# Kernel optimization log

Measured on AMD Instinct MI355X. Metric: run time of the kernel, lower is better.

Reference implementation:

```python
import jax, jax.numpy as jnp
import numpy as np

FEATS = 1024
HEAD = 16
MLP_HIDDEN = 4096
HEAD_DIM = FEATS // HEAD
SQRT_D = float(FEATS) ** 0.5  # module scales by sqrt(feats), not sqrt(head_dim)
LN_EPS = 1e-5


def layer_norm(x, g, b):
    mu = jnp.mean(x, axis=-1, keepdims=True)
    var = jnp.mean(jnp.square(x - mu), axis=-1, keepdims=True)
    return (x - mu) * jax.lax.rsqrt(var + LN_EPS) * g + b


def setup_inputs() -> dict:
    key = jax.random.key(0)
    ks = jax.random.split(key, 12)
    s = 1.0 / np.sqrt(FEATS)
    s2 = 1.0 / np.sqrt(MLP_HIDDEN)
    return {
        "x": jax.random.normal(ks[0], (2, 2048, FEATS), dtype=jnp.float32),
        "ln1_g": jnp.ones((FEATS,), jnp.float32),
        "ln1_b": jnp.zeros((FEATS,), jnp.float32),
        "wq": jax.random.normal(ks[1], (FEATS, FEATS), jnp.float32) * s,
        "bq": jnp.zeros((FEATS,), jnp.float32),
        "wk": jax.random.normal(ks[2], (FEATS, FEATS), jnp.float32) * s,
        "bk": jnp.zeros((FEATS,), jnp.float32),
        "wv": jax.random.normal(ks[3], (FEATS, FEATS), jnp.float32) * s,
        "bv": jnp.zeros((FEATS,), jnp.float32),
        "wo": jax.random.normal(ks[4], (FEATS, FEATS), jnp.float32) * s,
        "bo": jnp.zeros((FEATS,), jnp.float32),
        "ln2_g": jnp.ones((FEATS,), jnp.float32),
        "ln2_b": jnp.zeros((FEATS,), jnp.float32),
        "w1": jax.random.normal(ks[5], (MLP_HIDDEN, FEATS), jnp.float32) * s,
        "b1": jnp.zeros((MLP_HIDDEN,), jnp.float32),
        "w2": jax.random.normal(ks[6], (FEATS, MLP_HIDDEN), jnp.float32) * s2,
        "b2": jnp.zeros((FEATS,), jnp.float32),
    }


def reference(x, ln1_g, ln1_b, wq, bq, wk, bk, wv, bv, wo, bo,
              ln2_g, ln2_b, w1, b1, w2, b2):
    b, n, f = x.shape
    h = layer_norm(x, ln1_g, ln1_b)
    # qkv projections (torch Linear: y = x @ W.T + b)
    q = (h @ wq.T + bq).reshape(b, n, HEAD, HEAD_DIM).transpose(0, 2, 1, 3)
    k = (h @ wk.T + bk).reshape(b, n, HEAD, HEAD_DIM).transpose(0, 2, 1, 3)
    v = (h @ wv.T + bv).reshape(b, n, HEAD, HEAD_DIM).transpose(0, 2, 1, 3)
    score = jax.nn.softmax(jnp.einsum('bhif,bhjf->bhij', q, k) / SQRT_D, axis=-1)
    attn = jnp.einsum('bhij,bhjf->bihf', score, v).reshape(b, n, f)
    o = attn @ wo.T + bo
    out1 = o + x
    h2 = layer_norm(out1, ln2_g, ln2_b)
    mlp = jax.nn.relu(jax.nn.relu(h2 @ w1.T + b1) @ w2.T + b2)
    return mlp + out1
```

## Files before the change

kernel.cpp:

```cpp
#include <hip/hip_runtime.h>
#include <hip/hip_bf16.h>

#define FEATS 1024
#define NH 16
#define HD 64
#define SEQ 2048
#define BATCH 2
#define MTOT (BATCH*SEQ)
#define MLPH 4096

typedef __attribute__((ext_vector_type(8))) short bf16x8;
typedef __attribute__((ext_vector_type(4))) float f32x4;

static_assert(sizeof(bf16x8) == 16, "bf16x8 must be 16B");

__device__ __forceinline__ unsigned short f2bf(float f) {
    unsigned int u = __float_as_uint(f);
    unsigned int lsb = (u >> 16) & 1u;
    u += 0x7fffu + lsb;
    return (unsigned short)(u >> 16);
}

#define ASYNC16(GP, LP) __builtin_amdgcn_global_load_lds( \
    (const __attribute__((address_space(1))) void*)(GP),  \
    (__attribute__((address_space(3))) void*)(LP), 16, 0, 0)

__global__ __launch_bounds__(256) void cvt_kernel(const float* __restrict__ src,
                                                  unsigned short* __restrict__ dst, int n) {
    int i = (blockIdx.x * 256 + threadIdx.x) * 4;
    if (i + 3 < n) {
        float4 v = *(const float4*)(src + i);
        ushort4 o;
        o.x = f2bf(v.x); o.y = f2bf(v.y); o.z = f2bf(v.z); o.w = f2bf(v.w);
        *(ushort4*)(dst + i) = o;
    }
}

__global__ __launch_bounds__(256) void concat3_kernel(const float* __restrict__ a,
                                                      const float* __restrict__ b,
                                                      const float* __restrict__ c,
                                                      float* __restrict__ o) {
    int i = blockIdx.x * 256 + threadIdx.x;
    float v = (i < 1024) ? a[i] : ((i < 2048) ? b[i - 1024] : c[i - 2048]);
    o[i] = v;
}

__global__ __launch_bounds__(256) void ln_kernel(const float* __restrict__ x,
                                                 const float* __restrict__ g,
                                                 const float* __restrict__ bta,
                                                 unsigned short* __restrict__ h) {
    __shared__ float red[8];
    const int row = blockIdx.x;
    const int t = threadIdx.x;
    const float* xr = x + (size_t)row * FEATS;
    float4 v = ((const float4*)xr)[t];
    float s  = v.x + v.y + v.z + v.w;
    float ss = v.x * v.x + v.y * v.y + v.z * v.z + v.w * v.w;
#pragma unroll
    for (int off = 1; off < 64; off <<= 1) {
        s  += __shfl_xor(s, off);
        ss += __shfl_xor(ss, off);
    }
    const int w = t >> 6;
    if ((t & 63) == 0) { red[w] = s; red[4 + w] = ss; }
    __syncthreads();
    s  = red[0] + red[1] + red[2] + red[3];
    ss = red[4] + red[5] + red[6] + red[7];
    const float mu  = s * (1.f / FEATS);
    const float var = ss * (1.f / FEATS) - mu * mu;
    const float rs  = rsqrtf(var + 1e-5f);
    float4 gv = ((const float4*)g)[t];
    float4 bv = ((const float4*)bta)[t];
    ushort4 ov;
    ov.x = f2bf((v.x - mu) * rs * gv.x + bv.x);
    ov.y = f2bf((v.y - mu) * rs * gv.y + bv.y);
    ov.z = f2bf((v.z - mu) * rs * gv.z + bv.z);
    ov.w = f2bf((v.w - mu) * rs * gv.w + bv.w);
    ((ushort4*)h)[(size_t)row * (FEATS / 4) + t] = ov;
}

template <bool RELU, bool ADD, bool OUTBF16>
__global__ __launch_bounds__(256, 3)
void gemm_kernel(const unsigned short* __restrict__ A,
                 const unsigned short* __restrict__ W,
                 const float* __restrict__ bias,
                 const float* __restrict__ addend,
                 void* __restrict__ outp,
                 int M, int N, int K, int gx) {
    __shared__ unsigned short lds[3][2][128 * 32];

    const int t = threadIdx.x;
    const int w = t >> 6, lane = t & 63;
    const int wr = w >> 1, wc = w & 1;
    const int li = lane & 15, lj = lane >> 4;

    const int nwg = gridDim.x;
    const int cpx = nwg >> 3;
    const int wg = blockIdx.x;
    const int swz = (wg & 7) * cpx + (wg >> 3);
    const int mb = (swz / gx) * 128, nb = (swz % gx) * 128;

    const int srow = lane >> 2, sc = (lane & 3) * 8;
    const unsigned short* gA = A + (size_t)(mb + w * 16 + srow) * K + sc;
    const unsigned short* gB = W + (size_t)(nb + w * 16 + srow) * K + sc;
    const size_t half = (size_t)64 * K;
    const int lbase = w * 512 + lane * 8;

    const int nt = K >> 5;

#define STAGE(BUF, K0)                                             \
    do {                                                           \
        unsigned short* la_ = &lds[BUF][0][lbase];                 \
        unsigned short* lb_ = &lds[BUF][1][lbase];                 \
        ASYNC16(gA + (K0), la_);                                   \
        ASYNC16(gA + half + (K0), la_ + 2048);                     \
        ASYNC16(gB + (K0), lb_);                                   \
        ASYNC16(gB + half + (K0), lb_ + 2048);                     \
    } while (0)

    STAGE(0, 0);
    STAGE(1, 32);
    asm volatile("s_waitcnt vmcnt(4)" ::: "memory");
    __builtin_amdgcn_s_barrier();

    f32x4 acc[4][4] = {};

    for (int i = 0; i < nt; ++i) {
        const int cur = i % 3;
        const unsigned short* Al = &lds[cur][0][0];
        const unsigned short* Bl = &lds[cur][1][0];

        bf16x8 af[4], bfr[4];
#pragma unroll
        for (int m = 0; m < 4; m++)
            af[m] = *(const bf16x8*)(Al + (wr * 64 + m * 16 + li) * 32 + lj * 8);
#pragma unroll
        for (int n = 0; n < 4; n++)
            bfr[n] = *(const bf16x8*)(Bl + (wc * 64 + n * 16 + li) * 32 + lj * 8);

        const int pf = i + 2 < nt;
        if (pf) STAGE((i + 2) % 3, (i + 2) * 32);

#pragma unroll
        for (int m = 0; m < 4; m++)
#pragma unroll
            for (int n = 0; n < 4; n++)
                acc[m][n] = __builtin_amdgcn_mfma_f32_16x16x32_bf16(af[m], bfr[n], acc[m][n], 0, 0, 0);

        if (i + 1 < nt) {
            if (pf) asm volatile("s_waitcnt vmcnt(4)" ::: "memory");
            else    asm volatile("s_waitcnt vmcnt(0)" ::: "memory");
            __builtin_amdgcn_s_barrier();
        }
    }
#undef STAGE

#pragma unroll
    for (int m = 0; m < 4; m++) {
#pragma unroll
        for (int n = 0; n < 4; n++) {
            const int col = nb + wc * 64 + n * 16 + li;
            const float bv = bias[col];
#pragma unroll
            for (int r = 0; r < 4; r++) {
                const int row = mb + wr * 64 + m * 16 + lj * 4 + r;
                float v = acc[m][n][r] + bv;
                if (RELU) v = fmaxf(v, 0.f);
                if (ADD)  v += addend[(size_t)row * N + col];
                if (OUTBF16)
                    ((unsigned short*)outp)[(size_t)row * N + col] = f2bf(v);
                else
                    ((float*)outp)[(size_t)row * N + col] = v;
            }
        }
    }
}

__global__ __launch_bounds__(256) void vtrans_kernel(const unsigned short* __restrict__ qkv,
                                                     unsigned short* __restrict__ vt) {
    constexpr int LDV = 68;
    __shared__ unsigned short Vl[64 * LDV];
    const int bh = blockIdx.x, st = blockIdx.y;
    const int b = bh >> 4, h = bh & 15;
    const int t = threadIdx.x;
    const unsigned short* src = qkv + (size_t)(b * SEQ + st * 64) * (3 * FEATS) + 2 * FEATS + h * HD;
#pragma unroll
    for (int i = 0; i < 2; i++) {
        int idx = t + i * 256;
        int r = idx >> 3, c = (idx & 7) * 8;
        *(bf16x8*)(Vl + r * LDV + c) = *(const bf16x8*)(src + (size_t)r * (3 * FEATS) + c);
    }
    __syncthreads();
    unsigned short* dst = vt + (size_t)bh * HD * SEQ + st * 64;
#pragma unroll
    for (int i = 0; i < 2; i++) {
        int idx = t + i * 256;
        int d = idx >> 3, s8 = (idx & 7) * 8;
        bf16x8 v;
#pragma unroll
        for (int j = 0; j < 8; j++) v[j] = Vl[(s8 + j) * LDV + d];
        *(bf16x8*)(dst + (size_t)d * SEQ + s8) = v;
    }
}

__global__ __launch_bounds__(512, 4)
void attn_kernel(const unsigned short* __restrict__ qkv,
                 const unsigned short* __restrict__ vt,
                 unsigned short* __restrict__ out) {
    constexpr int LK = 72;
    constexpr int LP = 68;
    __shared__ unsigned short Kl[2][64 * LK];
    __shared__ unsigned short Vtl[2][64 * LK];
    __shared__ unsigned short Pl[8][16 * LP];

    const int bh = blockIdx.x;
    const int b = bh >> 4, h = bh & 15;
    const int q0 = blockIdx.y * 128;
    const int t = threadIdx.x, w = t >> 6, lane = t & 63;
    const int li = lane & 15, lj = lane >> 4;

    const size_t rstr = 3 * FEATS;
    const unsigned short* qkvb = qkv + (size_t)(b * SEQ) * rstr;
    const unsigned short* ksrc = qkvb + FEATS + h * HD;
    const unsigned short* vsrc = vt + (size_t)bh * HD * SEQ;

    bf16x8 aq[2];
#pragma unroll
    for (int kk = 0; kk < 2; kk++)
        aq[kk] = *(const bf16x8*)(qkvb + (size_t)(q0 + w * 16 + li) * rstr + h * HD + kk * 32 + lj * 8);

    f32x4 o[4] = {};
    float lsum[4] = {0.f, 0.f, 0.f, 0.f};
    const float c2 = 1.4426950408889634f / 32.0f;

    const int sr = t >> 3, scol = (t & 7) * 8;
    const unsigned short* kg = ksrc + (size_t)sr * rstr + scol;
    const unsigned short* vg = vsrc + (size_t)sr * SEQ + scol;
    const int ldo = sr * LK + scol;

    const int nt = SEQ / 64;

    {
        bf16x8 k0 = *(const bf16x8*)kg;
        bf16x8 v0 = *(const bf16x8*)vg;
        *(bf16x8*)(&Kl[0][ldo])  = k0;
        *(bf16x8*)(&Vtl[0][ldo]) = v0;
    }

    int cur = 0;
    for (int i = 0; i < nt; ++i) {
        bf16x8 kreg, vreg;
        if (i + 1 < nt) {
            kreg = *(const bf16x8*)(kg + (size_t)(i + 1) * 64 * rstr);
            vreg = *(const bf16x8*)(vg + (i + 1) * 64);
        }

        asm volatile("s_waitcnt lgkmcnt(0)" ::: "memory");
        __builtin_amdgcn_s_barrier();

        const unsigned short* Kc = Kl[cur];
        const unsigned short* Vc = Vtl[cur];

        f32x4 s[4];
        __builtin_amdgcn_s_setprio(1);
#pragma unroll
        for (int n = 0; n < 4; n++) {
            bf16x8 b0 = *(const bf16x8*)(Kc + (n * 16 + li) * LK + lj * 8);
            bf16x8 b1 = *(const bf16x8*)(Kc + (n * 16 + li) * LK + 32 + lj * 8);
            f32x4 acc = {};
            acc = __builtin_amdgcn_mfma_f32_16x16x32_bf16(aq[0], b0, acc, 0, 0, 0);
            acc = __builtin_amdgcn_mfma_f32_16x16x32_bf16(aq[1], b1, acc, 0, 0, 0);
            s[n] = acc;
        }
        __builtin_amdgcn_s_setprio(0);

#pragma unroll
        for (int n = 0; n < 4; n++)
#pragma unroll
            for (int r = 0; r < 4; r++) {
                float p = exp2f(s[n][r] * c2);
                lsum[r] += p;
                Pl[w][(lj * 4 + r) * LP + n * 16 + li] = f2bf(p);
            }

        __builtin_amdgcn_s_setprio(1);
#pragma unroll
        for (int kk = 0; kk < 2; kk++) {
            bf16x8 ap = *(const bf16x8*)(Pl[w] + li * LP + kk * 32 + lj * 8);
#pragma unroll
            for (int n = 0; n < 4; n++) {
                bf16x8 bv = *(const bf16x8*)(Vc + (n * 16 + li) * LK + kk * 32 + lj * 8);
                o[n] = __builtin_amdgcn_mfma_f32_16x16x32_bf16(ap, bv, o[n], 0, 0, 0);
            }
        }
        __builtin_amdgcn_s_setprio(0);

        if (i + 1 < nt) {
            *(bf16x8*)(&Kl[cur ^ 1][ldo])  = kreg;
            *(bf16x8*)(&Vtl[cur ^ 1][ldo]) = vreg;
        }
        cur ^= 1;
    }

    float inv[4];
#pragma unroll
    for (int r = 0; r < 4; r++) {
        float sred = lsum[r];
        sred += __shfl_xor(sred, 1);
        sred += __shfl_xor(sred, 2);
        sred += __shfl_xor(sred, 4);
        sred += __shfl_xor(sred, 8);
        inv[r] = 1.f / sred;
    }
    unsigned short* ob = out + (size_t)(b * SEQ + q0 + w * 16) * FEATS + h * HD;
#pragma unroll
    for (int n = 0; n < 4; n++)
#pragma unroll
        for (int r = 0; r < 4; r++)
            ob[(size_t)(lj * 4 + r) * FEATS + n * 16 + li] = f2bf(o[n][r] * inv[r]);
}

extern "C" void kernel_launch(void* const* d_in, const int* in_sizes, int n_in,
                              void* d_out, int out_size, void* d_ws, size_t ws_size,
                              hipStream_t stream) {
    const float* x     = (const float*)d_in[0];
    const float* ln1_g = (const float*)d_in[1];
    const float* ln1_b = (const float*)d_in[2];
    const float* wq    = (const float*)d_in[3];
    const float* bq    = (const float*)d_in[4];
    const float* wk    = (const float*)d_in[5];
    const float* bk    = (const float*)d_in[6];
    const float* wv    = (const float*)d_in[7];
    const float* bvv   = (const float*)d_in[8];
    const float* wo    = (const float*)d_in[9];
    const float* bo    = (const float*)d_in[10];
    const float* ln2_g = (const float*)d_in[11];
    const float* ln2_b = (const float*)d_in[12];
    const float* w1    = (const float*)d_in[13];
    const float* b1    = (const float*)d_in[14];
    const float* w2    = (const float*)d_in[15];
    const float* b2    = (const float*)d_in[16];

    unsigned short* wqkv_b = (unsigned short*)d_ws;
    unsigned short* wo_b   = wqkv_b + 3072 * 1024;
    unsigned short* w1_b   = wo_b + 1024 * 1024;
    unsigned short* w2_b   = w1_b + 4096 * 1024;
    float*          bqkv   = (float*)(w2_b + 1024 * 4096);
    unsigned short* region = (unsigned short*)(bqkv + 3072);
    unsigned short* qkvb   = region;
    unsigned short* hb     = region + (size_t)4096 * 3072;
    unsigned short* vtb    = hb;
    unsigned short* a1     = region;
    unsigned short* attn_o = region + (size_t)4096 * 4096;
    unsigned short* h2     = attn_o;
    float*          out1   = (float*)(attn_o + (size_t)4096 * 1024);
    float*          outf   = (float*)d_out;

    dim3 blk(256);

    cvt_kernel<<<1024, blk, 0, stream>>>(wq, wqkv_b, 1024 * 1024);
    cvt_kernel<<<1024, blk, 0, stream>>>(wk, wqkv_b + 1024 * 1024, 1024 * 1024);
    cvt_kernel<<<1024, blk, 0, stream>>>(wv, wqkv_b + 2 * 1024 * 1024, 1024 * 1024);
    cvt_kernel<<<1024, blk, 0, stream>>>(wo, wo_b, 1024 * 1024);
    cvt_kernel<<<4096, blk, 0, stream>>>(w1, w1_b, 4096 * 1024);
    cvt_kernel<<<4096, blk, 0, stream>>>(w2, w2_b, 4096 * 1024);
    concat3_kernel<<<12, blk, 0, stream>>>(bq, bk, bvv, bqkv);

    ln_kernel<<<MTOT, blk, 0, stream>>>(x, ln1_g, ln1_b, hb);

    gemm_kernel<false, false, true><<<768, blk, 0, stream>>>(
        hb, wqkv_b, bqkv, nullptr, qkvb, MTOT, 3072, FEATS, 24);

    vtrans_kernel<<<dim3(BATCH * NH, SEQ / 64), blk, 0, stream>>>(qkvb, vtb);

    attn_kernel<<<dim3(BATCH * NH, SEQ / 128), dim3(512), 0, stream>>>(qkvb, vtb, attn_o);

    gemm_kernel<false, true, false><<<256, blk, 0, stream>>>(
        attn_o, wo_b, bo, x, out1, MTOT, FEATS, FEATS, 8);

    ln_kernel<<<MTOT, blk, 0, stream>>>(out1, ln2_g, ln2_b, h2);

    gemm_kernel<true, false, true><<<1024, blk, 0, stream>>>(
        h2, w1_b, b1, nullptr, a1, MTOT, MLPH, FEATS, 32);

    gemm_kernel<true, true, false><<<256, blk, 0, stream>>>(
        a1, w2_b, b2, out1, outf, MTOT, FEATS, MLPH, 8);
}
```

Before: 259.9 us.

## Keep softmax probabilities in registers via transposed QK MFMA and permuted V layout

```diff
diff --git a/kernel.cpp b/kernel.cpp
--- a/kernel.cpp
+++ b/kernel.cpp
@@ -10,6 +10,7 @@
 #define MLPH 4096
 
 typedef __attribute__((ext_vector_type(8))) short bf16x8;
+typedef __attribute__((ext_vector_type(4))) short bf16x4;
 typedef __attribute__((ext_vector_type(4))) float f32x4;
 
 static_assert(sizeof(bf16x8) == 16, "bf16x8 must be 16B");
@@ -208,10 +209,8 @@
                  const unsigned short* __restrict__ vt,
                  unsigned short* __restrict__ out) {
     constexpr int LK = 72;
-    constexpr int LP = 68;
     __shared__ unsigned short Kl[2][64 * LK];
     __shared__ unsigned short Vtl[2][64 * LK];
-    __shared__ unsigned short Pl[8][16 * LP];
 
     const int bh = blockIdx.x;
     const int b = bh >> 4, h = bh & 15;
@@ -230,21 +229,26 @@
         aq[kk] = *(const bf16x8*)(qkvb + (size_t)(q0 + w * 16 + li) * rstr + h * HD + kk * 32 + lj * 8);
 
     f32x4 o[4] = {};
-    float lsum[4] = {0.f, 0.f, 0.f, 0.f};
+    float lsum = 0.f;
     const float c2 = 1.4426950408889634f / 32.0f;
 
     const int sr = t >> 3, scol = (t & 7) * 8;
     const unsigned short* kg = ksrc + (size_t)sr * rstr + scol;
     const unsigned short* vg = vsrc + (size_t)sr * SEQ + scol;
-    const int ldo = sr * LK + scol;
+    const int ldoK = sr * LK + scol;
+    const int posA = (scol & 32) + ((scol & 8) << 1) + ((scol & 16) >> 2);
+    const int ldoV = sr * LK + posA;
 
     const int nt = SEQ / 64;
 
     {
         bf16x8 k0 = *(const bf16x8*)kg;
         bf16x8 v0 = *(const bf16x8*)vg;
-        *(bf16x8*)(&Kl[0][ldo])  = k0;
-        *(bf16x8*)(&Vtl[0][ldo]) = v0;
+        *(bf16x8*)(&Kl[0][ldoK]) = k0;
+        bf16x4 vlo = __builtin_shufflevector(v0, v0, 0, 1, 2, 3);
+        bf16x4 vhi = __builtin_shufflevector(v0, v0, 4, 5, 6, 7);
+        *(bf16x4*)(&Vtl[0][ldoV])     = vlo;
+        *(bf16x4*)(&Vtl[0][ldoV + 8]) = vhi;
     }
 
     int cur = 0;
@@ -265,53 +269,60 @@
         __builtin_amdgcn_s_setprio(1);
 #pragma unroll
         for (int n = 0; n < 4; n++) {
-            bf16x8 b0 = *(const bf16x8*)(Kc + (n * 16 + li) * LK + lj * 8);
-            bf16x8 b1 = *(const bf16x8*)(Kc + (n * 16 + li) * LK + 32 + lj * 8);
+            bf16x8 k0 = *(const bf16x8*)(Kc + (n * 16 + li) * LK + lj * 8);
+            bf16x8 k1 = *(const bf16x8*)(Kc + (n * 16 + li) * LK + 32 + lj * 8);
             f32x4 acc = {};
-            acc = __builtin_amdgcn_mfma_f32_16x16x32_bf16(aq[0], b0, acc, 0, 0, 0);
-            acc = __builtin_amdgcn_mfma_f32_16x16x32_bf16(aq[1], b1, acc, 0, 0, 0);
+            acc = __builtin_amdgcn_mfma_f32_16x16x32_bf16(k0, aq[0], acc, 0, 0, 0);
+            acc = __builtin_amdgcn_mfma_f32_16x16x32_bf16(k1, aq[1], acc, 0, 0, 0);
             s[n] = acc;
         }
         __builtin_amdgcn_s_setprio(0);
 
+        float p[4][4];
 #pragma unroll
         for (int n = 0; n < 4; n++)
 #pragma unroll
             for (int r = 0; r < 4; r++) {
-                float p = exp2f(s[n][r] * c2);
-                lsum[r] += p;
-                Pl[w][(lj * 4 + r) * LP + n * 16 + li] = f2bf(p);
+                p[n][r] = exp2f(s[n][r] * c2);
+                lsum += p[n][r];
             }
+        union { unsigned u[4]; bf16x8 v; } A0u, A1u;
+#pragma unroll
+        for (int n = 0; n < 2; n++) {
+            asm("v_cvt_pk_bf16_f32 %0, %1, %2" : "=v"(A0u.u[n * 2])     : "v"(p[n][0]), "v"(p[n][1]));
+            asm("v_cvt_pk_bf16_f32 %0, %1, %2" : "=v"(A0u.u[n * 2 + 1]) : "v"(p[n][2]), "v"(p[n][3]));
+            asm("v_cvt_pk_bf16_f32 %0, %1, %2" : "=v"(A1u.u[n * 2])     : "v"(p[n + 2][0]), "v"(p[n + 2][1]));
+            asm("v_cvt_pk_bf16_f32 %0, %1, %2" : "=v"(A1u.u[n * 2 + 1]) : "v"(p[n + 2][2]), "v"(p[n + 2][3]));
+        }
 
         __builtin_amdgcn_s_setprio(1);
 #pragma unroll
-        for (int kk = 0; kk < 2; kk++) {
-            bf16x8 ap = *(const bf16x8*)(Pl[w] + li * LP + kk * 32 + lj * 8);
-#pragma unroll
-            for (int n = 0; n < 4; n++) {
-                bf16x8 bv = *(const bf16x8*)(Vc + (n * 16 + li) * LK + kk * 32 + lj * 8);
-                o[n] = __builtin_amdgcn_mfma_f32_16x16x32_bf16(ap, bv, o[n], 0, 0, 0);
-            }
+        for (int n = 0; n < 4; n++) {
+            bf16x8 bv0 = *(const bf16x8*)(Vc + (n * 16 + li) * LK + lj * 8);
+            bf16x8 bv1 = *(const bf16x8*)(Vc + (n * 16 + li) * LK + 32 + lj * 8);
+            o[n] = __builtin_amdgcn_mfma_f32_16x16x32_bf16(A0u.v, bv0, o[n], 0, 0, 0);
+            o[n] = __builtin_amdgcn_mfma_f32_16x16x32_bf16(A1u.v, bv1, o[n], 0, 0, 0);
         }
         __builtin_amdgcn_s_setprio(0);
 
         if (i + 1 < nt) {
-            *(bf16x8*)(&Kl[cur ^ 1][ldo])  = kreg;
-            *(bf16x8*)(&Vtl[cur ^ 1][ldo]) = vreg;
+            *(bf16x8*)(&Kl[cur ^ 1][ldoK]) = kreg;
+            bf16x4 vlo = __builtin_shufflevector(vreg, vreg, 0, 1, 2, 3);
+            bf16x4 vhi = __builtin_shufflevector(vreg, vreg, 4, 5, 6, 7);
+            *(bf16x4*)(&Vtl[cur ^ 1][ldoV])     = vlo;
+            *(bf16x4*)(&Vtl[cur ^ 1][ldoV + 8]) = vhi;
         }
         cur ^= 1;
     }
 
+    lsum += __shfl_xor(lsum, 16);
+    lsum += __shfl_xor(lsum, 32);
+    const float dinv = 1.f / lsum;
     float inv[4];
 #pragma unroll
-    for (int r = 0; r < 4; r++) {
-        float sred = lsum[r];
-        sred += __shfl_xor(sred, 1);
-        sred += __shfl_xor(sred, 2);
-        sred += __shfl_xor(sred, 4);
-        sred += __shfl_xor(sred, 8);
-        inv[r] = 1.f / sred;
-    }
+    for (int r = 0; r < 4; r++)
+        inv[r] = __shfl(dinv, lj * 4 + r);
+
     unsigned short* ob = out + (size_t)(b * SEQ + q0 + w * 16) * FEATS + h * HD;
 #pragma unroll
     for (int n = 0; n < 4; n++)
```

Result: faster. 249.4 us (-4.1%).
